# Optimization experiments

Measured on AMD Instinct MI355X. Metric: run time of the kernel, lower is better.

## Reference

```python
import jax, jax.numpy as jnp
import numpy as np
import math

B, T, D = 2, 2048, 1024
H, NL, DF = 16, 6, 4096
HD = D // H
EPS = 1e-5

def layer_norm(x, w, b):
    mu = jnp.mean(x, axis=-1, keepdims=True)
    var = jnp.mean((x - mu) ** 2, axis=-1, keepdims=True)
    return (x - mu) * jax.lax.rsqrt(var + EPS) * w + b

def setup_inputs() -> dict:
    key = jax.random.key(0)
    ks = jax.random.split(key, 12)
    def w(k, shape, scale=0.02):
        return jax.random.normal(k, shape, dtype=jnp.float32) * scale
    inp = {
        'sequences': jax.random.normal(ks[0], (B, T, D), dtype=jnp.float32),
        'Wq': w(ks[1], (NL, D, D)), 'bq': jnp.zeros((NL, D), jnp.float32),
        'Wk': w(ks[2], (NL, D, D)), 'bk': jnp.zeros((NL, D), jnp.float32),
        'Wv': w(ks[3], (NL, D, D)), 'bv': jnp.zeros((NL, D), jnp.float32),
        'Wo': w(ks[4], (NL, D, D)), 'bo': jnp.zeros((NL, D), jnp.float32),
        'Wz': w(ks[5], (NL, D, D)), 'bz': jnp.zeros((NL, D), jnp.float32),
        'Wr': w(ks[6], (NL, D, D)), 'br': jnp.zeros((NL, D), jnp.float32),
        'W1': w(ks[7], (NL, D, DF)), 'b1': jnp.zeros((NL, DF), jnp.float32),
        'W2': w(ks[8], (NL, DF, D)), 'b2': jnp.zeros((NL, D), jnp.float32),
        'ln1_w': jnp.ones((NL, D), jnp.float32), 'ln1_b': jnp.zeros((NL, D), jnp.float32),
        'ln2_w': jnp.ones((NL, D), jnp.float32), 'ln2_b': jnp.zeros((NL, D), jnp.float32),
        'lnf_w': jnp.ones((D,), jnp.float32), 'lnf_b': jnp.zeros((D,), jnp.float32),
    }
    return inp

def reference(sequences, Wq, bq, Wk, bk, Wv, bv, Wo, bo, Wz, bz, Wr, br,
              W1, b1, W2, b2, ln1_w, ln1_b, ln2_w, ln2_b, lnf_w, lnf_b):
    scale = 1.0 / math.sqrt(HD)
    causal = jnp.tril(jnp.ones((T, T), dtype=bool))  # mask[L:L+T, :L+T] with L=0
    x = sequences
    src = x
    for i in range(NL):
        xn = layer_norm(x, ln1_w[i], ln1_b[i])
        # QKV -> [B, H, T, HD]
        q = (xn @ Wq[i] + bq[i]).reshape(B, T, H, HD).transpose(0, 2, 1, 3)
        k = (xn @ Wk[i] + bk[i]).reshape(B, T, H, HD).transpose(0, 2, 1, 3)
        v = (xn @ Wv[i] + bv[i]).reshape(B, T, H, HD).transpose(0, 2, 1, 3)
        att = jnp.einsum('bhqd,bhkd->bhqk', q, k) * scale
        att = jnp.where(causal, att, -jnp.inf)
        att = jax.nn.softmax(att, axis=-1)
        y = jnp.einsum('bhqk,bhkd->bhqd', att, v)
        y = y.transpose(0, 2, 1, 3).reshape(B, T, D)
        x_attn = y @ Wo[i] + bo[i]
        z = jax.nn.sigmoid(xn @ Wz[i] + bz[i])
        r = jax.nn.sigmoid(xn @ Wr[i] + br[i])
        h_tilde = jnp.tanh(r * x_attn)
        x = (1.0 - z) * x + z * h_tilde
        xm = layer_norm(x, ln2_w[i], ln2_b[i])
        mlp = jax.nn.gelu(xm @ W1[i] + b1[i], approximate=False) @ W2[i] + b2[i]
        x = (1.0 - z) * x + z * mlp
        x = x + src
    x = layer_norm(x, lnf_w, lnf_b)
    return x
```

## Files before the change

kernel.cpp:

```cpp
#include <hip/hip_runtime.h>
#include <hip/hip_bf16.h>
#include <math.h>

#define B_ 2
#define T_ 2048
#define D_ 1024
#define H_ 16
#define NL_ 6
#define DF_ 4096
#define HD_ 64
#define M_ (B_*T_)

typedef __bf16 bf16;
typedef __attribute__((ext_vector_type(8))) __bf16 bf16x8;
typedef __attribute__((ext_vector_type(4))) float f32x4;
typedef __attribute__((ext_vector_type(16))) float f32x16;
typedef __attribute__((ext_vector_type(4))) unsigned u32x4;

#define BAR() __builtin_amdgcn_s_barrier()
#define LGKM0() asm volatile("s_waitcnt lgkmcnt(0)" ::: "memory")
#define VMC(n) asm volatile("s_waitcnt vmcnt(" #n ")" ::: "memory")

__device__ __forceinline__ void gload_lds16(const void* g, void* l) {
    __builtin_amdgcn_global_load_lds((const __attribute__((address_space(1))) void*)g,
                                     (__attribute__((address_space(3))) void*)l, 16, 0, 0);
}

__device__ __forceinline__ unsigned pk2(float a, float b) {
    bf16 lo = (bf16)a, hb = (bf16)b;
    return (unsigned)__builtin_bit_cast(unsigned short, lo) |
           ((unsigned)__builtin_bit_cast(unsigned short, hb) << 16);
}

template<bool OUT_BF16>
__global__ __launch_bounds__(256) void ln_kernel(const float* __restrict__ x,
        const float* __restrict__ w, const float* __restrict__ b,
        void* __restrict__ out) {
    const int row = blockIdx.x;
    const int t = threadIdx.x;
    const float4 xv = *(const float4*)(x + (long)row * D_ + t * 4);
    float s  = xv.x + xv.y + xv.z + xv.w;
    float sq = xv.x*xv.x + xv.y*xv.y + xv.z*xv.z + xv.w*xv.w;
    #pragma unroll
    for (int m = 32; m; m >>= 1) { s += __shfl_xor(s, m); sq += __shfl_xor(sq, m); }
    __shared__ float red[8];
    const int wid = t >> 6, lid = t & 63;
    if (lid == 0) { red[wid] = s; red[wid + 4] = sq; }
    __syncthreads();
    s  = red[0] + red[1] + red[2] + red[3];
    sq = red[4] + red[5] + red[6] + red[7];
    const float mu   = s * (1.0f / D_);
    const float var  = sq * (1.0f / D_) - mu * mu;
    const float rstd = rsqrtf(var + 1e-5f);
    const float4 wv = *(const float4*)(w + t * 4);
    const float4 bv = *(const float4*)(b + t * 4);
    float o0 = (xv.x - mu) * rstd * wv.x + bv.x;
    float o1 = (xv.y - mu) * rstd * wv.y + bv.y;
    float o2 = (xv.z - mu) * rstd * wv.z + bv.z;
    float o3 = (xv.w - mu) * rstd * wv.w + bv.w;
    if (OUT_BF16) {
        bf16* o = (bf16*)out + (long)row * D_ + t * 4;
        o[0] = (bf16)o0; o[1] = (bf16)o1; o[2] = (bf16)o2; o[3] = (bf16)o3;
    } else {
        float* o = (float*)out + (long)row * D_ + t * 4;
        o[0] = o0; o[1] = o1; o[2] = o2; o[3] = o3;
    }
}

__global__ __launch_bounds__(256) void wconv_all(
        const float* __restrict__ Wq, const float* __restrict__ Wk,
        const float* __restrict__ Wv, const float* __restrict__ Wz,
        const float* __restrict__ Wr, const float* __restrict__ Wo,
        const float* __restrict__ W1, const float* __restrict__ W2,
        bf16* __restrict__ wt) {
    __shared__ float s[32][33];
    const int bid = blockIdx.x;
    const float* src; bf16* dst; int t, K, nlg;
    if (bid < 6144) {
        const int m = bid >> 10; t = bid & 1023; K = 1024; nlg = 5;
        switch (m) {
            case 0: src = Wq; dst = wt; break;
            case 1: src = Wk; dst = wt + (1u << 20); break;
            case 2: src = Wv; dst = wt + (2u << 20); break;
            case 3: src = Wz; dst = wt + (3u << 20); break;
            case 4: src = Wr; dst = wt + (4u << 20); break;
            default: src = Wo; dst = wt + (5u << 20); break;
        }
    } else if (bid < 10240) {
        t = bid - 6144; K = 1024; nlg = 7; src = W1; dst = wt + (6u << 20);
    } else {
        t = bid - 10240; K = 4096; nlg = 5; src = W2; dst = wt + (10u << 20);
    }
    const int N = 1 << (nlg + 5);
    const int k0 = (t >> nlg) * 32, n0 = (t & ((1 << nlg) - 1)) * 32;
    const int c = threadIdx.x & 31, r8 = threadIdx.x >> 5;
    #pragma unroll
    for (int it = 0; it < 4; it++)
        s[r8 + it*8][c] = src[(long)(k0 + r8 + it*8) * N + n0 + c];
    __syncthreads();
    #pragma unroll
    for (int it = 0; it < 4; it++)
        dst[(long)(n0 + r8 + it*8) * K + k0 + c] = (bf16)s[c][r8 + it*8];
}

#define MFMA16(a, b, c) __builtin_amdgcn_mfma_f32_16x16x32_bf16(a, b, c, 0, 0, 0)
#define MFMA32(a, b, c) __builtin_amdgcn_mfma_f32_32x32x16_bf16(a, b, c, 0, 0, 0)

__device__ __forceinline__ void gemm128_core(const bf16* __restrict__ A, const bf16* __restrict__ Bt,
        const int Ks, const int NT, const int m0, const int n0, char* lds, f32x4 (&acc)[4][4]) {
    const int tid = threadIdx.x;
    const int lane = tid & 63, w = tid >> 6;
    const int wm = w >> 1, wn = w & 1;
    const int cl = lane & 15, gl = lane >> 4;
    const int srow = lane >> 2;
    const int sxc = (((lane & 3) ^ (srow & 3)) << 3);
    const bf16* pa0 = A  + (size_t)(m0 + w * 32 + srow) * Ks + sxc;
    const bf16* pa1 = pa0 + (size_t)16 * Ks;
    const bf16* pb  = Bt + (size_t)(n0 + w * 16 + srow) * Ks + sxc;
    char* laA = lds + w * 2048;
    char* laB = lds + 32768 + w * 1024;

#define STG(KT, BUF) do { \
    gload_lds16(pa0 + (size_t)(KT) * 32, laA + (BUF) * 16384); \
    gload_lds16(pa1 + (size_t)(KT) * 32, laA + (BUF) * 16384 + 1024); \
    gload_lds16(pb  + (size_t)(KT) * 32, laB + (BUF) * 8192); } while (0)

    STG(0, 0); STG(1, 1);
    VMC(3);
    BAR();

    const int xo  = ((gl ^ (cl & 3)) << 4);
    const int rdA = (wm * 64 + cl) * 64 + xo;
    const int rdB = (wn * 64 + cl) * 64 + xo;

    for (int kt = 0; kt < NT; ++kt) {
        const int buf = kt & 1;
        const char* sA = lds + buf * 16384;
        const char* sB = lds + 32768 + buf * 8192;
        bf16x8 a[4], b[4];
        #pragma unroll
        for (int mi = 0; mi < 4; mi++) a[mi] = *(const bf16x8*)(sA + rdA + mi * 1024);
        #pragma unroll
        for (int ni = 0; ni < 4; ni++) b[ni] = *(const bf16x8*)(sB + rdB + ni * 1024);
        BAR(); LGKM0();
        __builtin_amdgcn_s_setprio(1);
        #pragma unroll
        for (int mi = 0; mi < 2; mi++)
            #pragma unroll
            for (int ni = 0; ni < 4; ni++)
                acc[mi][ni] = MFMA16(a[mi], b[ni], acc[mi][ni]);
        __builtin_amdgcn_s_setprio(0);
        BAR();
        if (kt + 2 < NT) STG(kt + 2, buf);
        __builtin_amdgcn_s_setprio(1);
        #pragma unroll
        for (int mi = 2; mi < 4; mi++)
            #pragma unroll
            for (int ni = 0; ni < 4; ni++)
                acc[mi][ni] = MFMA16(a[mi], b[ni], acc[mi][ni]);
        __builtin_amdgcn_s_setprio(0);
        if (kt + 2 < NT)      { VMC(3); }
        else if (kt + 1 < NT) { VMC(0); }
        BAR();
    }
#undef STG
}

__global__ __launch_bounds__(512, 4) void gemm5_k(const bf16* __restrict__ A, const bf16* __restrict__ Bt,
        const float* __restrict__ bq, const float* __restrict__ bk, const float* __restrict__ bvv,
        const float* __restrict__ bz, const float* __restrict__ br,
        bf16* __restrict__ oq, bf16* __restrict__ ok, bf16* __restrict__ ov,
        float* __restrict__ oz, float* __restrict__ orr) {
    __shared__ __align__(16) char lds[49152];
    int bid = blockIdx.x;
    bid = (bid & 7) * 80 + (bid >> 3);
    const int m0 = (bid / 40) * 256, n0 = (bid % 40) * 128;
    f32x4 acc[4][4];
    #pragma unroll
    for (int i = 0; i < 4; i++)
        #pragma unroll
        for (int j = 0; j < 4; j++) acc[i][j] = (f32x4){0.f, 0.f, 0.f, 0.f};
    gemm128_core(A, Bt, 1024, 32, m0, n0, lds, acc);
    const int tid = threadIdx.x, lane = tid & 63, w = tid >> 6;
    const int wm = w >> 1, wn = w & 1, cl = lane & 15, gl = lane >> 4;
    const int seg = n0 >> 10;
    const int lc0 = (n0 & 1023) + wn * 64;
    const float* bias; int mode; void* outp;
    switch (seg) {
        case 0:  bias = bq;  mode = 0; outp = oq;  break;
        case 1:  bias = bk;  mode = 0; outp = ok;  break;
        case 2:  bias = bvv; mode = 1; outp = ov;  break;
        case 3:  bias = bz;  mode = 2; outp = oz;  break;
        default: bias = br;  mode = 2; outp = orr; break;
    }
    const float scl = (seg == 0) ? 0.125f : 1.0f;
    #pragma unroll
    for (int mi = 0; mi < 4; mi++) {
        #pragma unroll
        for (int ni = 0; ni < 4; ni++) {
            const int lcol = lc0 + ni * 16 + cl;
            const float bv = bias[lcol];
            #pragma unroll
            for (int r = 0; r < 4; r++) {
                const int row = m0 + wm * 64 + mi * 16 + gl * 4 + r;
                const float v = (acc[mi][ni][r] + bv) * scl;
                if (mode == 0) {
                    ((bf16*)outp)[(long)row * 1024 + lcol] = (bf16)v;
                } else if (mode == 1) {
                    ((bf16*)outp)[((long)(row >> 11) * 1024 + lcol) * T_ + (row & 2047)] = (bf16)v;
                } else {
                    ((float*)outp)[(long)row * 1024 + lcol] = 1.0f / (1.0f + __expf(-v));
                }
            }
        }
    }
}

__global__ __launch_bounds__(512, 4) void gemmG_k(const bf16* __restrict__ A, const bf16* __restrict__ Bt,
        const float* __restrict__ bias, bf16* __restrict__ out) {
    __shared__ __align__(16) char lds[49152];
    int bid = blockIdx.x;
    bid = (bid & 7) * 64 + (bid >> 3);
    const int m0 = (bid >> 5) * 256, n0 = (bid & 31) * 128;
    f32x4 acc[4][4];
    #pragma unroll
    for (int i = 0; i < 4; i++)
        #pragma unroll
        for (int j = 0; j < 4; j++) acc[i][j] = (f32x4){0.f, 0.f, 0.f, 0.f};
    gemm128_core(A, Bt, 1024, 32, m0, n0, lds, acc);
    const int tid = threadIdx.x, lane = tid & 63, w = tid >> 6;
    const int wm = w >> 1, wn = w & 1, cl = lane & 15, gl = lane >> 4;
    #pragma unroll
    for (int mi = 0; mi < 4; mi++) {
        #pragma unroll
        for (int ni = 0; ni < 4; ni++) {
            const int col = n0 + wn * 64 + ni * 16 + cl;
            const float bv = bias[col];
            #pragma unroll
            for (int r = 0; r < 4; r++) {
                const int row = m0 + wm * 64 + mi * 16 + gl * 4 + r;
                float v = acc[mi][ni][r] + bv;
                v = 0.5f * v * (1.0f + erff(v * 0.70710678118f));
                out[(long)row * DF_ + col] = (bf16)v;
            }
        }
    }
}

__global__ __launch_bounds__(512, 4) void gemmP_k(const bf16* __restrict__ A, const bf16* __restrict__ Bt,
        float* __restrict__ p0, float* __restrict__ p1, float* __restrict__ p2, float* __restrict__ p3) {
    __shared__ __align__(16) char lds[49152];
    int bid = blockIdx.x;
    bid = (bid & 7) * 64 + (bid >> 3);
    const int mt = bid >> 5, s = (bid >> 3) & 3, ntl = bid & 7;
    const int m0 = mt * 256, n0 = ntl * 128;
    f32x4 acc[4][4];
    #pragma unroll
    for (int i = 0; i < 4; i++)
        #pragma unroll
        for (int j = 0; j < 4; j++) acc[i][j] = (f32x4){0.f, 0.f, 0.f, 0.f};
    gemm128_core(A + s * 1024, Bt + s * 1024, 4096, 32, m0, n0, lds, acc);
    float* outp = (s == 0) ? p0 : (s == 1) ? p1 : (s == 2) ? p2 : p3;
    const int tid = threadIdx.x, lane = tid & 63, w = tid >> 6;
    const int wm = w >> 1, wn = w & 1, cl = lane & 15, gl = lane >> 4;
    #pragma unroll
    for (int mi = 0; mi < 4; mi++) {
        #pragma unroll
        for (int ni = 0; ni < 4; ni++) {
            const int col = n0 + wn * 64 + ni * 16 + cl;
            #pragma unroll
            for (int r = 0; r < 4; r++) {
                const int row = m0 + wm * 64 + mi * 16 + gl * 4 + r;
                outp[(long)row * 1024 + col] = acc[mi][ni][r];
            }
        }
    }
}

__global__ __launch_bounds__(256) void gemmWo_kernel(const bf16* __restrict__ A,
        const bf16* __restrict__ Bt, const float* __restrict__ bias,
        float* __restrict__ out) {
    __shared__ bf16 sA[128 * 32];
    __shared__ bf16 sB[128 * 32];
    const int tid = threadIdx.x;
    int bid = blockIdx.x;
    bid = (bid & 7) * 32 + (bid >> 3);
    const int m0 = (bid >> 3) * 128, n0 = (bid & 7) * 128;
    f32x4 acc[4][4];
    #pragma unroll
    for (int i = 0; i < 4; i++)
        #pragma unroll
        for (int j = 0; j < 4; j++) acc[i][j] = (f32x4){0.f, 0.f, 0.f, 0.f};
    const int lane = tid & 63, w = tid >> 6;
    const int wr = (w >> 1) * 64, wc = (w & 1) * 64;
    const int cl = lane & 15, gl = lane >> 4;
    const int srow = tid >> 2, skoff = (tid & 3) * 8;
    const bf16* ga = A  + (long)(m0 + srow) * D_ + skoff;
    const bf16* gb = Bt + (long)(n0 + srow) * D_ + skoff;
    char* sAc = (char*)sA;
    char* sBc = (char*)sB;
    const int wb = w * 1024;
    for (int k0 = 0; k0 < D_; k0 += 32) {
        if (k0) __syncthreads();
        gload_lds16(ga + k0,            sAc + wb);
        gload_lds16(ga + 64 * D_ + k0,  sAc + 4096 + wb);
        gload_lds16(gb + k0,            sBc + wb);
        gload_lds16(gb + 64 * D_ + k0,  sBc + 4096 + wb);
        __syncthreads();
        bf16x8 af[4], bfr[4];
        #pragma unroll
        for (int i = 0; i < 4; i++) af[i]  = *(const bf16x8*)(sA + (wr + i*16 + cl) * 32 + 8 * gl);
        #pragma unroll
        for (int j = 0; j < 4; j++) bfr[j] = *(const bf16x8*)(sB + (wc + j*16 + cl) * 32 + 8 * gl);
        #pragma unroll
        for (int i = 0; i < 4; i++)
            #pragma unroll
            for (int j = 0; j < 4; j++)
                acc[i][j] = MFMA16(af[i], bfr[j], acc[i][j]);
    }
    #pragma unroll
    for (int i = 0; i < 4; i++) {
        #pragma unroll
        for (int j = 0; j < 4; j++) {
            const int gcol = n0 + wc + j * 16 + cl;
            const float bv = bias[gcol];
            #pragma unroll
            for (int r = 0; r < 4; r++) {
                const int grow = m0 + wr + i * 16 + gl * 4 + r;
                out[(long)grow * D_ + gcol] = acc[i][j][r] + bv;
            }
        }
    }
}

__global__ __launch_bounds__(256, 2) void attn_kernel(const bf16* __restrict__ q,
        const bf16* __restrict__ k, const bf16* __restrict__ vT,
        bf16* __restrict__ y) {
    __shared__ __align__(16) char lds[32768];
    const int tid = threadIdx.x, wid = tid >> 6, lane = tid & 63;
    const int col = lane & 31, hi = lane >> 5;
    const int bid = blockIdx.x;
    const int xcd = bid & 7, idx = bid >> 3;
    const int bh = xcd + 8 * (idx & 3);
    const int sg = idx >> 2;
    const int g = (sg & 1) ? (sg >> 1) : (15 - (sg >> 1));
    const int qt = 4 * g + wid;
    const int qb = qt * 32;
    const int b = bh >> 4, h = bh & 15;
    const int NP = 2 * g + 2;
    const int nt64 = (qt >> 1) + 1;

    const bf16* qB = q  + (size_t)b * T_ * D_ + h * HD_;
    const bf16* kB = k  + (size_t)b * T_ * D_ + h * HD_;
    const bf16* vB = vT + (size_t)b * D_ * T_ + (size_t)h * HD_ * T_;

    const int sr = wid * 8 + (lane >> 3);
    const int sc = lane & 7;
    const bf16* kS0 = kB + (size_t)sr * D_ + 8 * (sc ^ (sr & 7));
    const bf16* kS1 = kS0 + (size_t)32 * D_;
    const bf16* vS0 = vB + (size_t)sr * T_ + 8 * (sc ^ (sr & 7));
    const bf16* vS1 = vS0 + (size_t)32 * T_;
    char* dK = lds + wid * 1024;
    char* dV = lds + 16384 + wid * 1024;

#define ASTG(J, BUF) do { \
    const size_t ko_ = (size_t)(J) * 64 * D_; \
    const size_t vo_ = (size_t)(J) * 64; \
    gload_lds16(kS0 + ko_, dK + (BUF) * 8192); \
    gload_lds16(kS1 + ko_, dK + (BUF) * 8192 + 4096); \
    gload_lds16(vS0 + vo_, dV + (BUF) * 8192); \
    gload_lds16(vS1 + vo_, dV + (BUF) * 8192 + 4096); } while (0)

    bf16x8 qf0, qf1, qf2, qf3;
    {
        const bf16* qp = qB + (size_t)(qb + col) * D_ + 8 * hi;
        qf0 = *(const bf16x8*)(qp);
        qf1 = *(const bf16x8*)(qp + 16);
        qf2 = *(const bf16x8*)(qp + 32);
        qf3 = *(const bf16x8*)(qp + 48);
    }

    f32x16 Od0, Od1;
    #pragma unroll
    for (int i = 0; i < 16; i++) { Od0[i] = 0.f; Od1[i] = 0.f; }
    float mrun = -INFINITY, lrun = 0.f;

    ASTG(0, 0);
    ASTG(1, 1);
    VMC(4);
    BAR();

    const int swz = col & 7;
    for (int j = 0; j < NP; ++j) {
        const int buf = j & 1;
        if (j < nt64) {
            const char* bK = lds + buf * 8192;
            const char* bV = lds + 16384 + buf * 8192;
            bf16x8 kf0[4], kf1[4], vf0[4], vf1[4];
            #pragma unroll
            for (int cs = 0; cs < 4; cs++) {
                const int ch = ((hi + 2 * cs) ^ swz) * 16;
                kf0[cs] = *(const bf16x8*)(bK + col * 128 + ch);
                kf1[cs] = *(const bf16x8*)(bK + (col + 32) * 128 + ch);
                vf0[cs] = *(const bf16x8*)(bV + col * 128 + ch);
                vf1[cs] = *(const bf16x8*)(bV + (col + 32) * 128 + ch);
            }
            f32x16 S0, S1;
            #pragma unroll
            for (int i = 0; i < 16; i++) { S0[i] = 0.f; S1[i] = 0.f; }
            S0 = MFMA32(kf0[0], qf0, S0); S0 = MFMA32(kf0[1], qf1, S0);
            S0 = MFMA32(kf0[2], qf2, S0); S0 = MFMA32(kf0[3], qf3, S0);
            S1 = MFMA32(kf1[0], qf0, S1); S1 = MFMA32(kf1[1], qf1, S1);
            S1 = MFMA32(kf1[2], qf2, S1); S1 = MFMA32(kf1[3], qf3, S1);
            float p[32];
            #pragma unroll
            for (int r = 0; r < 16; r++) { p[r] = S0[r]; p[16 + r] = S1[r]; }
            if (j == nt64 - 1) {
                const int qr = qb + col;
                #pragma unroll
                for (int r = 0; r < 32; r++) {
                    const int kvl = 64 * j + 32 * (r >> 4)
                                  + (r & 3) + 8 * ((r & 15) >> 2) + 4 * hi;
                    if (kvl > qr) p[r] = -3.0e38f;
                }
            }
            float tm = p[0];
            #pragma unroll
            for (int r = 1; r < 32; r++) tm = fmaxf(tm, p[r]);
            tm = fmaxf(tm, __shfl_xor(tm, 32));
            if (!__all(tm <= mrun + 8.f)) {
                const float mn = fmaxf(mrun, tm);
                const float al = __expf(mrun - mn);
                lrun *= al;
                #pragma unroll
                for (int i = 0; i < 16; i++) { Od0[i] *= al; Od1[i] *= al; }
                mrun = mn;
            }
            float ts = 0.f;
            #pragma unroll
            for (int r = 0; r < 32; r++) { p[r] = __expf(p[r] - mrun); ts += p[r]; }
            ts += __shfl_xor(ts, 32);
            lrun += ts;
            bf16x8 pbf[4];
            #pragma unroll
            for (int t = 0; t < 2; t++) {
                const unsigned pw0 = pk2(p[16*t+0],  p[16*t+1]),  pw1 = pk2(p[16*t+2],  p[16*t+3]);
                const unsigned pw2 = pk2(p[16*t+4],  p[16*t+5]),  pw3 = pk2(p[16*t+6],  p[16*t+7]);
                const unsigned pw4 = pk2(p[16*t+8],  p[16*t+9]),  pw5 = pk2(p[16*t+10], p[16*t+11]);
                const unsigned pw6 = pk2(p[16*t+12], p[16*t+13]), pw7 = pk2(p[16*t+14], p[16*t+15]);
                const unsigned px0 = __shfl_xor((int)pw0, 32), px1 = __shfl_xor((int)pw1, 32);
                const unsigned px2 = __shfl_xor((int)pw2, 32), px3 = __shfl_xor((int)pw3, 32);
                const unsigned px4 = __shfl_xor((int)pw4, 32), px5 = __shfl_xor((int)pw5, 32);
                const unsigned px6 = __shfl_xor((int)pw6, 32), px7 = __shfl_xor((int)pw7, 32);
                const u32x4 c0 = hi ? (u32x4){px2, px3, pw2, pw3} : (u32x4){pw0, pw1, px0, px1};
                const u32x4 c1 = hi ? (u32x4){px6, px7, pw6, pw7} : (u32x4){pw4, pw5, px4, px5};
                pbf[2*t]   = __builtin_bit_cast(bf16x8, c0);
                pbf[2*t+1] = __builtin_bit_cast(bf16x8, c1);
            }
            #pragma unroll
            for (int f = 0; f < 4; f++) {
                Od0 = MFMA32(vf0[f], pbf[f], Od0);
                Od1 = MFMA32(vf1[f], pbf[f], Od1);
            }
        }
        BAR();
        if (j + 2 < NP) { ASTG(j + 2, buf); VMC(4); }
        else            { VMC(0); }
        BAR();
    }

    const float inv = 1.0f / lrun;
    bf16* yr = y + (size_t)(b * T_ + qb + col) * D_ + h * HD_;
    #pragma unroll
    for (int rg = 0; rg < 4; rg++) {
        const int d0 = 8 * rg + 4 * hi;
        uint2 s0 = { pk2(Od0[4*rg] * inv, Od0[4*rg+1] * inv), pk2(Od0[4*rg+2] * inv, Od0[4*rg+3] * inv) };
        *(uint2*)(yr + d0) = s0;
        uint2 s1 = { pk2(Od1[4*rg] * inv, Od1[4*rg+1] * inv), pk2(Od1[4*rg+2] * inv, Od1[4*rg+3] * inv) };
        *(uint2*)(yr + 32 + d0) = s1;
    }
#undef ASTG
}

__global__ __launch_bounds__(256) void gate1_kernel(float* __restrict__ x,
        const float* __restrict__ z, const float* __restrict__ r,
        const float* __restrict__ xa) {
    const long i = ((long)blockIdx.x * 256 + threadIdx.x) * 4;
    float4 xv = *(const float4*)(x + i);
    const float4 zv = *(const float4*)(z + i);
    const float4 rv = *(const float4*)(r + i);
    const float4 av = *(const float4*)(xa + i);
    xv.x = (1.f - zv.x) * xv.x + zv.x * tanhf(rv.x * av.x);
    xv.y = (1.f - zv.y) * xv.y + zv.y * tanhf(rv.y * av.y);
    xv.z = (1.f - zv.z) * xv.z + zv.z * tanhf(rv.z * av.z);
    xv.w = (1.f - zv.w) * xv.w + zv.w * tanhf(rv.w * av.w);
    *(float4*)(x + i) = xv;
}

__global__ __launch_bounds__(256) void gate2_kernel(float* __restrict__ x,
        const float* __restrict__ z,
        const float* __restrict__ p0, const float* __restrict__ p1,
        const float* __restrict__ p2, const float* __restrict__ p3,
        const float* __restrict__ src, const float* __restrict__ b2) {
    const long i = ((long)blockIdx.x * 256 + threadIdx.x) * 4;
    float4 xv = *(const float4*)(x + i);
    const float4 zv = *(const float4*)(z + i);
    const float4 a0 = *(const float4*)(p0 + i);
    const float4 a1 = *(const float4*)(p1 + i);
    const float4 a2 = *(const float4*)(p2 + i);
    const float4 a3 = *(const float4*)(p3 + i);
    const float4 sv = *(const float4*)(src + i);
    const float4 bb = *(const float4*)(b2 + (i & 1023));
    const float mx = a0.x + a1.x + a2.x + a3.x + bb.x;
    const float my = a0.y + a1.y + a2.y + a3.y + bb.y;
    const float mz = a0.z + a1.z + a2.z + a3.z + bb.z;
    const float mw = a0.w + a1.w + a2.w + a3.w + bb.w;
    xv.x = (1.f - zv.x) * xv.x + zv.x * mx + sv.x;
    xv.y = (1.f - zv.y) * xv.y + zv.y * my + sv.y;
    xv.z = (1.f - zv.z) * xv.z + zv.z * mz + sv.z;
    xv.w = (1.f - zv.w) * xv.w + zv.w * mw + sv.w;
    *(float4*)(x + i) = xv;
}

extern "C" void kernel_launch(void* const* d_in, const int* in_sizes, int n_in,
                              void* d_out, int out_size, void* d_ws, size_t ws_size,
                              hipStream_t stream) {
    const float* seq   = (const float*)d_in[0];
    const float* Wq    = (const float*)d_in[1];  const float* bq = (const float*)d_in[2];
    const float* Wk    = (const float*)d_in[3];  const float* bk = (const float*)d_in[4];
    const float* Wv    = (const float*)d_in[5];  const float* bv = (const float*)d_in[6];
    const float* Wo    = (const float*)d_in[7];  const float* bo = (const float*)d_in[8];
    const float* Wz    = (const float*)d_in[9];  const float* bz = (const float*)d_in[10];
    const float* Wr    = (const float*)d_in[11]; const float* br = (const float*)d_in[12];
    const float* W1    = (const float*)d_in[13]; const float* b1 = (const float*)d_in[14];
    const float* W2    = (const float*)d_in[15]; const float* b2 = (const float*)d_in[16];
    const float* ln1w  = (const float*)d_in[17]; const float* ln1b = (const float*)d_in[18];
    const float* ln2w  = (const float*)d_in[19]; const float* ln2b = (const float*)d_in[20];
    const float* lnfw  = (const float*)d_in[21]; const float* lnfb = (const float*)d_in[22];

    char* ws = (char*)d_ws;
    float* x   = (float*)(ws);
    float* z   = (float*)(ws + ((size_t)16 << 20));
    float* r   = (float*)(ws + ((size_t)32 << 20));
    float* xa  = (float*)(ws + ((size_t)48 << 20));
    bf16*  xn  = (bf16*)(ws + ((size_t)64 << 20));
    bf16*  qb_ = (bf16*)(ws + ((size_t)72 << 20));
    bf16*  kb_ = (bf16*)(ws + ((size_t)80 << 20));
    bf16*  vtb = (bf16*)(ws + ((size_t)88 << 20));
    bf16*  yb  = (bf16*)(ws + ((size_t)96 << 20));
    bf16*  h1  = (bf16*)(ws + ((size_t)104 << 20));
    bf16*  wt  = (bf16*)(ws + ((size_t)136 << 20));
    float* pt2 = (float*)(ws + ((size_t)172 << 20));
    float* pt3 = (float*)(ws + ((size_t)188 << 20));

    bf16* wto = wt + (5u << 20);
    bf16* wt1 = wt + (6u << 20);
    bf16* wt2 = wt + (10u << 20);

    hipMemcpyAsync(x, seq, (size_t)M_ * D_ * 4, hipMemcpyDeviceToDevice, stream);

    for (int i = 0; i < NL_; i++) {
        const long dd = (long)i * D_ * D_;
        wconv_all<<<14336, 256, 0, stream>>>(Wq + dd, Wk + dd, Wv + dd, Wz + dd,
                                             Wr + dd, Wo + dd,
                                             W1 + (long)i * D_ * DF_,
                                             W2 + (long)i * DF_ * D_, wt);
        ln_kernel<true><<<M_, 256, 0, stream>>>(x, ln1w + i * D_, ln1b + i * D_, xn);
        gemm5_k<<<640, 512, 0, stream>>>(xn, wt,
                bq + i * D_, bk + i * D_, bv + i * D_, bz + i * D_, br + i * D_,
                qb_, kb_, vtb, z, r);
        attn_kernel<<<512, 256, 0, stream>>>(qb_, kb_, vtb, yb);
        gemmWo_kernel<<<256, 256, 0, stream>>>(yb, wto, bo + i * D_, xa);
        gate1_kernel<<<(M_ * D_) / 1024, 256, 0, stream>>>(x, z, r, xa);
        ln_kernel<true><<<M_, 256, 0, stream>>>(x, ln2w + i * D_, ln2b + i * D_, xn);
        gemmG_k<<<512, 512, 0, stream>>>(xn, wt1, b1 + i * DF_, h1);
        gemmP_k<<<512, 512, 0, stream>>>(h1, wt2, xa, r, pt2, pt3);
        gate2_kernel<<<(M_ * D_) / 1024, 256, 0, stream>>>(x, z, xa, r, pt2, pt3, seq, b2 + i * D_);
    }
    ln_kernel<false><<<M_, 256, 0, stream>>>(x, lnfw, lnfb, d_out);
}
```

Measured before the change: 1.795 ms.

## Fuse first GRU gate into Wo GEMM epilogue and fix LDS swizzle

Moves the first gating update (tanh of r times attention output, blended into x by z) into the Wo GEMM epilogue and deletes the separate gate1 kernel. This drops the fp32 xa round trip through memory and one launch per layer. The LDS XOR swizzle in gemm128_core also changes to use bits 1-2 of the row, and the same swizzle is added to the Wo GEMM to cut bank conflicts. The fused epilogue does scalar, strided loads of z, r and x instead of float4 loads. The xa buffer is still passed to gemmP_k, but there it appears to be reused as scratch.

```diff
diff --git a/kernel.cpp b/kernel.cpp
--- a/kernel.cpp
+++ b/kernel.cpp
@@ -113,7 +113,7 @@
     const int wm = w >> 1, wn = w & 1;
     const int cl = lane & 15, gl = lane >> 4;
     const int srow = lane >> 2;
-    const int sxc = (((lane & 3) ^ (srow & 3)) << 3);
+    const int sxc = (((lane & 3) ^ ((lane >> 3) & 3)) << 3);
     const bf16* pa0 = A  + (size_t)(m0 + w * 32 + srow) * Ks + sxc;
     const bf16* pa1 = pa0 + (size_t)16 * Ks;
     const bf16* pb  = Bt + (size_t)(n0 + w * 16 + srow) * Ks + sxc;
@@ -129,7 +129,7 @@
     VMC(3);
     BAR();
 
-    const int xo  = ((gl ^ (cl & 3)) << 4);
+    const int xo  = ((gl ^ ((cl >> 1) & 3)) << 4);
     const int rdA = (wm * 64 + cl) * 64 + xo;
     const int rdB = (wn * 64 + cl) * 64 + xo;
 
@@ -277,9 +277,9 @@
     }
 }
 
-__global__ __launch_bounds__(256) void gemmWo_kernel(const bf16* __restrict__ A,
+__global__ __launch_bounds__(256) void gemmWoG_kernel(const bf16* __restrict__ A,
         const bf16* __restrict__ Bt, const float* __restrict__ bias,
-        float* __restrict__ out) {
+        float* __restrict__ x, const float* __restrict__ z, const float* __restrict__ rr) {
     __shared__ bf16 sA[128 * 32];
     __shared__ bf16 sB[128 * 32];
     const int tid = threadIdx.x;
@@ -294,12 +294,14 @@
     const int lane = tid & 63, w = tid >> 6;
     const int wr = (w >> 1) * 64, wc = (w & 1) * 64;
     const int cl = lane & 15, gl = lane >> 4;
-    const int srow = tid >> 2, skoff = (tid & 3) * 8;
+    const int srow = tid >> 2;
+    const int skoff = (((tid & 3) ^ ((tid >> 3) & 3)) << 3);
     const bf16* ga = A  + (long)(m0 + srow) * D_ + skoff;
     const bf16* gb = Bt + (long)(n0 + srow) * D_ + skoff;
     char* sAc = (char*)sA;
     char* sBc = (char*)sB;
     const int wb = w * 1024;
+    const int xo = ((gl ^ ((cl >> 1) & 3)) << 4);
     for (int k0 = 0; k0 < D_; k0 += 32) {
         if (k0) __syncthreads();
         gload_lds16(ga + k0,            sAc + wb);
@@ -309,9 +311,9 @@
         __syncthreads();
         bf16x8 af[4], bfr[4];
         #pragma unroll
-        for (int i = 0; i < 4; i++) af[i]  = *(const bf16x8*)(sA + (wr + i*16 + cl) * 32 + 8 * gl);
-        #pragma unroll
-        for (int j = 0; j < 4; j++) bfr[j] = *(const bf16x8*)(sB + (wc + j*16 + cl) * 32 + 8 * gl);
+        for (int i = 0; i < 4; i++) af[i]  = *(const bf16x8*)(sAc + (wr + i*16 + cl) * 64 + xo);
+        #pragma unroll
+        for (int j = 0; j < 4; j++) bfr[j] = *(const bf16x8*)(sBc + (wc + j*16 + cl) * 64 + xo);
         #pragma unroll
         for (int i = 0; i < 4; i++)
             #pragma unroll
@@ -327,7 +329,11 @@
             #pragma unroll
             for (int r = 0; r < 4; r++) {
                 const int grow = m0 + wr + i * 16 + gl * 4 + r;
-                out[(long)grow * D_ + gcol] = acc[i][j][r] + bv;
+                const long idx = (long)grow * D_ + gcol;
+                const float xa = acc[i][j][r] + bv;
+                const float zv = z[idx];
+                const float ht = tanhf(rr[idx] * xa);
+                x[idx] = (1.f - zv) * x[idx] + zv * ht;
             }
         }
     }
@@ -480,21 +486,6 @@
         *(uint2*)(yr + 32 + d0) = s1;
     }
 #undef ASTG
-}
-
-__global__ __launch_bounds__(256) void gate1_kernel(float* __restrict__ x,
-        const float* __restrict__ z, const float* __restrict__ r,
-        const float* __restrict__ xa) {
-    const long i = ((long)blockIdx.x * 256 + threadIdx.x) * 4;
-    float4 xv = *(const float4*)(x + i);
-    const float4 zv = *(const float4*)(z + i);
-    const float4 rv = *(const float4*)(r + i);
-    const float4 av = *(const float4*)(xa + i);
-    xv.x = (1.f - zv.x) * xv.x + zv.x * tanhf(rv.x * av.x);
-    xv.y = (1.f - zv.y) * xv.y + zv.y * tanhf(rv.y * av.y);
-    xv.z = (1.f - zv.z) * xv.z + zv.z * tanhf(rv.z * av.z);
-    xv.w = (1.f - zv.w) * xv.w + zv.w * tanhf(rv.w * av.w);
-    *(float4*)(x + i) = xv;
 }
 
 __global__ __launch_bounds__(256) void gate2_kernel(float* __restrict__ x,
@@ -570,8 +561,7 @@
                 bq + i * D_, bk + i * D_, bv + i * D_, bz + i * D_, br + i * D_,
                 qb_, kb_, vtb, z, r);
         attn_kernel<<<512, 256, 0, stream>>>(qb_, kb_, vtb, yb);
-        gemmWo_kernel<<<256, 256, 0, stream>>>(yb, wto, bo + i * D_, xa);
-        gate1_kernel<<<(M_ * D_) / 1024, 256, 0, stream>>>(x, z, r, xa);
+        gemmWoG_kernel<<<256, 256, 0, stream>>>(yb, wto, bo + i * D_, x, z, r);
         ln_kernel<true><<<M_, 256, 0, stream>>>(x, ln2w + i * D_, ln2b + i * D_, xn);
         gemmG_k<<<512, 512, 0, stream>>>(xn, wt1, b1 + i * DF_, h1);
         gemmP_k<<<512, 512, 0, stream>>>(h1, wt2, xa, r, pt2, pt3);
```

Measured after the change: 1.793 ms. No clear change (-0.1%).
